# Performance work log

Measured on AMD Instinct MI355X. Metric: run time of the kernel, lower is better.

## Reference

```python
import jax, jax.numpy as jnp
import numpy as np

B, L, D = 4, 4096, 64

def setup_inputs() -> dict:
    key = jax.random.key(0)
    k1, k2, k3, k4 = jax.random.split(key, 4)
    return {
        "query": jax.random.normal(k1, (B, L, D), dtype=jnp.float32),
        "key": jax.random.normal(k2, (B, L, D), dtype=jnp.float32),
        "value": jax.random.normal(k3, (B, L, D), dtype=jnp.float32),
        "mask": jax.random.uniform(k4, (B, L, L), dtype=jnp.float32),
        "d_k": D,
    }

def reference(query, key, value, mask, d_k):
    # scores: [B, Lq, Lk] = Q @ K^T / sqrt(d_k), then multiplicative mask
    scale = 1.0 / jnp.sqrt(jnp.asarray(d_k, dtype=query.dtype))
    scores = jnp.einsum("bqd,bkd->bqk", query, key) * scale * mask
    attn = jax.nn.softmax(scores, axis=-1)  # row-wise over keys
    return jnp.einsum("bqk,bkd->bqd", attn, value)
```

## Files before the change

### kernel.cpp

```cpp
#include <hip/hip_runtime.h>
#include <hip/hip_bf16.h>
#include <stdint.h>
#include <stddef.h>

#define B_   4
#define L_   4096
#define D_   64
#define TK_  64
#define NKT  (L_/TK_)
#define TQ_  64
#define NQB  (L_/TQ_)
#define KROW 144

typedef __attribute__((ext_vector_type(8))) short bf16x8;
typedef __attribute__((ext_vector_type(4))) float f32x4;
typedef __attribute__((ext_vector_type(4))) unsigned short u16x4;

__device__ static inline unsigned short f2bf(float x) {
  union { __hip_bfloat16 h; unsigned short u; } cv;
  cv.h = __float2bfloat16(x);
  return cv.u;
}

__global__ __launch_bounds__(256) void attn_fused(
    const float* __restrict__ Q, const float* __restrict__ K,
    const float* __restrict__ V, const float* __restrict__ Mk,
    float* __restrict__ out) {
  __shared__ char Kbuf[2][TK_*KROW];
  __shared__ char Vbuf[2][TK_*KROW];
  __shared__ char Pbuf[4][16*KROW];

  const int idx = blockIdx.x;
  const int b   = (idx & 7) >> 1;
  const int qt  = ((idx >> 3) << 1) | (idx & 1);

  const int tid  = threadIdx.x;
  const int w    = tid >> 6;
  const int lane = tid & 63;
  const int i16  = lane & 15;
  const int quad = lane >> 4;
  const int q0   = qt*TQ_ + w*16;

  const int dq = tid & 15;
  const int kq = tid >> 4;

  const float cs = 0.125f * 1.44269504088896f;
  bf16x8 aq[2];
  {
    const float* qp = Q + ((size_t)b*L_ + q0 + i16)*D_ + quad*8;
#pragma unroll
    for (int ks=0; ks<2; ++ks) {
      const f32x4* p = (const f32x4*)(qp + ks*32);
      f32x4 x0 = p[0], x1 = p[1];
      bf16x8 v;
      for (int j=0;j<4;++j) v[j]   = (short)f2bf(x0[j]*cs);
      for (int j=0;j<4;++j) v[4+j] = (short)f2bf(x1[j]*cs);
      aq[ks] = v;
    }
  }

  const float* mbase = Mk + ((size_t)b*L_ + q0 + quad*4)*(size_t)L_ + 4*i16;
  const float* kbase = K + ((size_t)b*L_ + kq*4)*D_ + dq*4;
  const float* vbase = V + ((size_t)b*L_ + kq*4)*D_ + dq*4;

  f32x4 O[4];
#pragma unroll
  for (int t=0;t<4;++t) O[t] = (f32x4){0.f,0.f,0.f,0.f};
  float l_acc[4] = {0.f,0.f,0.f,0.f};
  f32x4 cmv[4], nmv[4];
  f32x4 kreg[4], vreg[4];

#pragma unroll
  for (int r=0;r<4;++r) {
    kreg[r] = *(const f32x4*)(kbase + (size_t)r*D_);
    vreg[r] = *(const f32x4*)(vbase + (size_t)r*D_);
    cmv[r]  = *(const f32x4*)(mbase + (size_t)r*L_);
  }
#pragma unroll
  for (int r=0;r<4;++r) nmv[r] = cmv[r];

  for (int kt=0; kt<NKT; ++kt) {
    const int buf = kt & 1;

    {
      char* kb = Kbuf[buf]; char* vb = Vbuf[buf];
#pragma unroll
      for (int r=0;r<4;++r) {
        u16x4 pk;
        for (int j=0;j<4;++j) pk[j] = f2bf(kreg[r][j]);
        *(u16x4*)(kb + (r*16+kq)*KROW + dq*8) = pk;
      }
#pragma unroll
      for (int e=0;e<4;++e) {
        u16x4 pv;
        for (int r=0;r<4;++r) pv[r] = f2bf(vreg[r][e]);
        *(u16x4*)(vb + (dq*4+e)*KROW + kq*8) = pv;
      }
    }
    __syncthreads();

    if (kt+1 < NKT) {
      const size_t roff = (size_t)(kt+1)*TK_*(size_t)D_;
      const size_t kc   = (size_t)(kt+1)*TK_;
#pragma unroll
      for (int r=0;r<4;++r) {
        kreg[r] = *(const f32x4*)(kbase + roff + (size_t)r*D_);
        vreg[r] = *(const f32x4*)(vbase + roff + (size_t)r*D_);
        nmv[r]  = *(const f32x4*)(mbase + (size_t)r*L_ + kc);
      }
    }

    f32x4 acc[4];
    const char* kb = Kbuf[buf];
#pragma unroll
    for (int t=0;t<4;++t) {
      acc[t] = (f32x4){0.f,0.f,0.f,0.f};
#pragma unroll
      for (int ks=0;ks<2;++ks) {
        bf16x8 bfr = *(const bf16x8*)(kb + (t*16+i16)*KROW + ks*64 + quad*16);
        acc[t] = __builtin_amdgcn_mfma_f32_16x16x32_bf16(aq[ks], bfr, acc[t], 0,0,0);
      }
    }

    float p[16]; float rs[4] = {0.f,0.f,0.f,0.f};
#pragma unroll
    for (int t=0;t<4;++t)
#pragma unroll
      for (int r=0;r<4;++r) {
        float v = __builtin_amdgcn_exp2f(acc[t][r] * cmv[r][t]);
        p[t*4+r] = v; rs[r] += v;
      }
#pragma unroll
    for (int r=0;r<4;++r) {
      float s = rs[r];
      s += __shfl_xor(s, 1); s += __shfl_xor(s, 2);
      s += __shfl_xor(s, 4); s += __shfl_xor(s, 8);
      l_acc[r] += s;
    }

    char* pb = Pbuf[w];
#pragma unroll
    for (int r=0;r<4;++r) {
      u16x4 pk;
      for (int t=0;t<4;++t) pk[t] = f2bf(p[t*4+r]);
      *(u16x4*)(pb + (quad*4+r)*KROW + i16*8) = pk;
    }

    const char* vb = Vbuf[buf];
#pragma unroll
    for (int ks=0;ks<2;++ks) {
      bf16x8 af = *(const bf16x8*)(pb + i16*KROW + ks*64 + quad*16);
#pragma unroll
      for (int dt=0;dt<4;++dt) {
        bf16x8 vf = *(const bf16x8*)(vb + (dt*16+i16)*KROW + ks*64 + quad*16);
        O[dt] = __builtin_amdgcn_mfma_f32_16x16x32_bf16(af, vf, O[dt], 0,0,0);
      }
    }

#pragma unroll
    for (int r=0;r<4;++r) cmv[r] = nmv[r];
  }

  float inv[4];
#pragma unroll
  for (int r=0;r<4;++r) inv[r] = 1.0f / l_acc[r];
#pragma unroll
  for (int t=0;t<4;++t)
#pragma unroll
    for (int r=0;r<4;++r)
      out[((size_t)b*L_ + q0 + quad*4 + r)*D_ + t*16 + i16] = O[t][r]*inv[r];
}

extern "C" void kernel_launch(void* const* d_in, const int* in_sizes, int n_in,
                              void* d_out, int out_size, void* d_ws, size_t ws_size,
                              hipStream_t stream) {
  const float* Q  = (const float*)d_in[0];
  const float* K  = (const float*)d_in[1];
  const float* V  = (const float*)d_in[2];
  const float* Mk = (const float*)d_in[3];
  (void)d_ws; (void)ws_size;

  attn_fused<<<B_*NQB, 256, 0, stream>>>(Q, K, V, Mk, (float*)d_out);
}
```

Baseline: 428.7 us.

## Split key sequence across two wave groups per block and merge partials

Doubles the block to 512 threads, with each half of the waves processing half of the key tiles for the same query rows, using separate double-buffered K/V shared tiles. At the end the second half writes its partial output and row sums to shared memory and the first half merges them and normalizes. This increases waves per CU to hide memory and MFMA latency in a grid that only has one block per CU, at the cost of more LDS and a final reduction step.

```diff
diff --git a/kernel.cpp b/kernel.cpp
--- a/kernel.cpp
+++ b/kernel.cpp
@@ -8,9 +8,11 @@
 #define D_   64
 #define TK_  64
 #define NKT  (L_/TK_)
+#define NKH  (NKT/2)
 #define TQ_  64
 #define NQB  (L_/TQ_)
 #define KROW 144
+#define TILE_BYTES (TK_*KROW)
 
 typedef __attribute__((ext_vector_type(8))) short bf16x8;
 typedef __attribute__((ext_vector_type(4))) float f32x4;
@@ -22,13 +24,13 @@
   return cv.u;
 }
 
-__global__ __launch_bounds__(256) void attn_fused(
+__global__ __launch_bounds__(512) void attn_fused(
     const float* __restrict__ Q, const float* __restrict__ K,
     const float* __restrict__ V, const float* __restrict__ Mk,
     float* __restrict__ out) {
-  __shared__ char Kbuf[2][TK_*KROW];
-  __shared__ char Vbuf[2][TK_*KROW];
-  __shared__ char Pbuf[4][16*KROW];
+  __shared__ char Kbuf[2][2][TILE_BYTES];
+  __shared__ char Vbuf[2][2][TILE_BYTES];
+  __shared__ char Pbuf[8][16*KROW];
 
   const int idx = blockIdx.x;
   const int b   = (idx & 7) >> 1;
@@ -36,13 +38,16 @@
 
   const int tid  = threadIdx.x;
   const int w    = tid >> 6;
+  const int qw   = w & 3;
+  const int half = w >> 2;
   const int lane = tid & 63;
   const int i16  = lane & 15;
   const int quad = lane >> 4;
-  const int q0   = qt*TQ_ + w*16;
-
-  const int dq = tid & 15;
-  const int kq = tid >> 4;
+  const int q0   = qt*TQ_ + qw*16;
+
+  const int st = tid & 255;
+  const int dq = st & 15;
+  const int kq = st >> 4;
 
   const float cs = 0.125f * 1.44269504088896f;
   bf16x8 aq[2];
@@ -59,9 +64,11 @@
     }
   }
 
-  const float* mbase = Mk + ((size_t)b*L_ + q0 + quad*4)*(size_t)L_ + 4*i16;
-  const float* kbase = K + ((size_t)b*L_ + kq*4)*D_ + dq*4;
-  const float* vbase = V + ((size_t)b*L_ + kq*4)*D_ + dq*4;
+  const float* mbase = Mk + ((size_t)b*L_ + q0 + quad*4)*(size_t)L_
+                          + half*(NKH*TK_) + 4*i16;
+  const size_t krow0 = (size_t)b*L_ + (size_t)half*(NKH*TK_) + kq*4;
+  const float* kbase = K + krow0*D_ + dq*4;
+  const float* vbase = V + krow0*D_ + dq*4;
 
   f32x4 O[4];
 #pragma unroll
@@ -79,11 +86,11 @@
 #pragma unroll
   for (int r=0;r<4;++r) nmv[r] = cmv[r];
 
-  for (int kt=0; kt<NKT; ++kt) {
+  for (int kt=0; kt<NKH; ++kt) {
     const int buf = kt & 1;
 
     {
-      char* kb = Kbuf[buf]; char* vb = Vbuf[buf];
+      char* kb = Kbuf[half][buf]; char* vb = Vbuf[half][buf];
 #pragma unroll
       for (int r=0;r<4;++r) {
         u16x4 pk;
@@ -99,7 +106,7 @@
     }
     __syncthreads();
 
-    if (kt+1 < NKT) {
+    if (kt+1 < NKH) {
       const size_t roff = (size_t)(kt+1)*TK_*(size_t)D_;
       const size_t kc   = (size_t)(kt+1)*TK_;
 #pragma unroll
@@ -111,7 +118,7 @@
     }
 
     f32x4 acc[4];
-    const char* kb = Kbuf[buf];
+    const char* kb = Kbuf[half][buf];
 #pragma unroll
     for (int t=0;t<4;++t) {
       acc[t] = (f32x4){0.f,0.f,0.f,0.f};
@@ -146,7 +153,7 @@
       *(u16x4*)(pb + (quad*4+r)*KROW + i16*8) = pk;
     }
 
-    const char* vb = Vbuf[buf];
+    const char* vb = Vbuf[half][buf];
 #pragma unroll
     for (int ks=0;ks<2;++ks) {
       bf16x8 af = *(const bf16x8*)(pb + i16*KROW + ks*64 + quad*16);
@@ -161,14 +168,34 @@
     for (int r=0;r<4;++r) cmv[r] = nmv[r];
   }
 
-  float inv[4];
-#pragma unroll
-  for (int r=0;r<4;++r) inv[r] = 1.0f / l_acc[r];
-#pragma unroll
-  for (int t=0;t<4;++t)
-#pragma unroll
-    for (int r=0;r<4;++r)
-      out[((size_t)b*L_ + q0 + quad*4 + r)*D_ + t*16 + i16] = O[t][r]*inv[r];
+  float* Ol = (float*)&Kbuf[0][0][0];
+  float* Ll = (float*)&Pbuf[0][0];
+  __syncthreads();
+  if (half == 1) {
+#pragma unroll
+    for (int t=0;t<4;++t)
+      *(f32x4*)&Ol[((size_t)qw*64 + t*16 + i16)*20 + quad*4] = O[t];
+    if (i16 == 0) {
+#pragma unroll
+      for (int r=0;r<4;++r) Ll[qw*16 + quad*4 + r] = l_acc[r];
+    }
+  }
+  __syncthreads();
+  if (half == 0) {
+#pragma unroll
+    for (int t=0;t<4;++t) {
+      f32x4 op = *(const f32x4*)&Ol[((size_t)qw*64 + t*16 + i16)*20 + quad*4];
+      O[t] += op;
+    }
+    float inv[4];
+#pragma unroll
+    for (int r=0;r<4;++r) inv[r] = 1.0f / (l_acc[r] + Ll[qw*16 + quad*4 + r]);
+#pragma unroll
+    for (int t=0;t<4;++t)
+#pragma unroll
+      for (int r=0;r<4;++r)
+        out[((size_t)b*L_ + q0 + quad*4 + r)*D_ + t*16 + i16] = O[t][r]*inv[r];
+  }
 }
 
 extern "C" void kernel_launch(void* const* d_in, const int* in_sizes, int n_in,
@@ -180,5 +207,5 @@
   const float* Mk = (const float*)d_in[3];
   (void)d_ws; (void)ws_size;
 
-  attn_fused<<<B_*NQB, 256, 0, stream>>>(Q, K, V, Mk, (float*)d_out);
+  attn_fused<<<B_*NQB, 512, 0, stream>>>(Q, K, V, Mk, (float*)d_out);
 }
```

New measurement: 407.5 us. 1.05x faster.
